# Optimization experiments

Measured on AMD Instinct MI355X. Metric: run time of the kernel, lower is better.

## Reference

```python
import jax, jax.numpy as jnp
import numpy as np

DT = 0.1
TAU = 100.0
ALPHA = DT / TAU


def setup_inputs() -> dict:
    key = jax.random.key(0)
    ks = jax.random.split(key, 4)
    seq_len, batch, in_size, hidden, out_size = 1024, 256, 128, 512, 32
    inputs = jax.random.normal(ks[0], (seq_len, batch, in_size), dtype=jnp.float32)
    W_rec = jax.random.normal(ks[1], (hidden, hidden), dtype=jnp.float32) / hidden ** 0.5
    W_in = jax.random.normal(ks[2], (in_size, hidden), dtype=jnp.float32) / in_size ** 0.5
    b_rec = jnp.zeros((hidden,), dtype=jnp.float32)
    W_out = jax.random.normal(ks[3], (hidden, out_size), dtype=jnp.float32) / hidden ** 0.5
    b_out = jnp.zeros((out_size,), dtype=jnp.float32)
    return {"inputs": inputs, "W_rec": W_rec, "W_in": W_in, "b_rec": b_rec,
            "W_out": W_out, "b_out": b_out}


def reference(inputs, W_rec, W_in, b_rec, W_out, b_out):
    # Precompute input projection for all timesteps: [T, B, H]
    x_proj = jnp.einsum('tbi,ih->tbh', inputs, W_in) + b_rec
    batch, hidden = inputs.shape[1], W_rec.shape[0]
    h0 = jnp.zeros((batch, hidden), dtype=inputs.dtype)

    def step(h, xp_t):
        # h @ W_rec.T matches torch's h @ self.W_rec.t()
        h_new = (1.0 - ALPHA) * h + ALPHA * jax.nn.relu(h @ W_rec.T + xp_t)
        return h_new, h_new

    _, hs = jax.lax.scan(step, h0, x_proj)  # hs: [T, B, H]
    outputs = jnp.einsum('tbh,ho->tbo', hs, W_out) + b_out
    return outputs
```

## Files before the change

### kernel.cpp

```cpp
#include <hip/hip_runtime.h>

typedef __attribute__((ext_vector_type(8))) short short8;
typedef __attribute__((ext_vector_type(4))) float floatx4;

#define T_STEPS 1024
#define BATCH   256
#define INSZ    128
#define HID     512
#define OUTSZ   32

#define MFMA16(a,b,c) __builtin_amdgcn_mfma_f32_16x16x32_bf16((a),(b),(c),0,0,0)

static __device__ __forceinline__ short f2bf(float f) {
  unsigned int u = __float_as_uint(f);
  u += 0x7fffu + ((u >> 16) & 1u);
  return (short)(u >> 16);
}
static __device__ __forceinline__ float bf2f(short s) {
  return __uint_as_float(((unsigned int)(unsigned short)s) << 16);
}
static __device__ __forceinline__ unsigned cvt_pk_bf16(float lo, float hi) {
  unsigned r;
  asm("v_cvt_pk_bf16_f32 %0, %1, %2" : "=v"(r) : "v"(lo), "v"(hi));
  return r;
}

__global__ __launch_bounds__(256) void pack_kernel(
    const float* __restrict__ W_rec, const float* __restrict__ W_in,
    const float* __restrict__ W_out,
    short* __restrict__ w_rec_p, short* __restrict__ w_in_p,
    short* __restrict__ w_out_p) {
  int i = blockIdx.x * 256 + threadIdx.x;
  {
    int n = i >> 9, k = i & 511;
    int pos = ((((k >> 5) * 32 + (n >> 4)) * 64 + ((k >> 3) & 3) * 16 + (n & 15)) << 3) + (k & 7);
    w_rec_p[pos] = f2bf(W_rec[i]);
  }
  if (i < INSZ * HID) {
    int k = i >> 9, n = i & 511;
    int pos = ((((k >> 5) * 32 + (n >> 4)) * 64 + ((k >> 3) & 3) * 16 + (n & 15)) << 3) + (k & 7);
    w_in_p[pos] = f2bf(W_in[i]);
  }
  if (i < HID * OUTSZ) {
    int k = i >> 5, o = i & 31;
    int pos = ((((k >> 5) * 2 + (o >> 4)) * 64 + ((k >> 3) & 3) * 16 + (o & 15)) << 3) + (k & 7);
    w_out_p[pos] = f2bf(W_out[i]);
  }
}

__global__ __launch_bounds__(512, 1) void fused_kernel(
    const float* __restrict__ inputs,
    const short* __restrict__ w_rec_p, const short* __restrict__ w_in_p,
    const short* __restrict__ w_out_p,
    const float* __restrict__ b_rec, const float* __restrict__ b_out,
    short* __restrict__ xp0, short* __restrict__ xp1,
    short* __restrict__ hs0, short* __restrict__ hs1,
    float* __restrict__ h_carry, float* __restrict__ out,
    unsigned long long* __restrict__ xch, unsigned* __restrict__ flags,
    int c, int chunk, int nchunks) {
  __shared__ __align__(16) char smem[163840];
  const int tid  = threadIdx.x;
  const int wave = tid >> 6, lane = tid & 63;
  const int l15  = lane & 15, q = lane >> 4;

  const int sb = (c >= 0 && c < nchunks) ? 32 : 0;
  const int nx = (c + 1 < nchunks) ? chunk : 0;
  const int bid = blockIdx.x;

  if (bid < sb) {
    short* w_lds = (short*)smem;
    short* hbuf  = (short*)(smem + 131072);
    const short* xp = (c & 1) ? xp1 : xp0;
    short* hs = (c & 1) ? hs1 : hs0;
    const int s    = bid;
    const int slab = s >> 1;
    const int ch   = s & 1;
    const int ps   = s ^ 1;
    const int first = (c == 0);

    short8 wreg[8][2];
    #pragma unroll
    for (int kt = 0; kt < 8; ++kt)
      #pragma unroll
      for (int i = 0; i < 2; ++i) {
        int ct = (ch << 4) + wave * 2 + i;
        wreg[kt][i] = *(const short8*)(w_rec_p + (((kt * 32 + ct) * 64 + lane) << 3));
      }

    for (int e = tid * 8; e < 8 * 16 * 512; e += 512 * 8) {
      int kt8 = e >> 13;
      int rest = e & 8191;
      *(short8*)(w_lds + e) =
          *(const short8*)(w_rec_p + ((8 + kt8) * 32 + (ch << 4)) * 512 + rest);
    }

    #pragma unroll
    for (int g4 = 0; g4 < 4; ++g4) {
      int col = (wave * 4 + g4) * 16 + l15;
      int ck = col >> 3, cl = col & 7;
      #pragma unroll
      for (int r = 0; r < 4; ++r) {
        int row = q * 4 + r;
        float v = first ? 0.f : h_carry[(size_t)(slab * 16 + row) * HID + col];
        hbuf[row * 512 + ((ck ^ row) << 3) + cl] = f2bf(v);
      }
    }
    float hold[2][4];
    #pragma unroll
    for (int i = 0; i < 2; ++i) {
      int col = (ch << 8) + wave * 32 + i * 16 + l15;
      #pragma unroll
      for (int r = 0; r < 4; ++r)
        hold[i][r] = first ? 0.f : h_carry[(size_t)(slab * 16 + q * 4 + r) * HID + col];
    }

    const float alpha = (float)(0.1 / 100.0);
    const float onem  = (float)(1.0 - 0.1 / 100.0);

    __syncthreads();

    int p = 0;
    for (int t = 0; t < chunk; ++t) {
      const int g = c * chunk + t;
      const short* hb = hbuf + p * (16 * 512);
      short* hnb = hbuf + (p ^ 1) * (16 * 512);

      uint2 xq[2];
      #pragma unroll
      for (int i = 0; i < 2; ++i)
        xq[i] = *(const uint2*)(xp + ((((size_t)t * 16 + slab) * 32 + (ch << 4) + wave * 2 + i) * 64 + lane) * 4);

      if (t > 0) {
        int e2 = tid * 16;
        int row = e2 >> 9, off = e2 & 511;
        int ck2 = (ch << 5) + (off >> 4);
        short8 v = *(const short8*)(hb + row * 512 + ((ck2 ^ row) << 3));
        *(short8*)(hs + ((size_t)(t - 1) * BATCH + slab * 16 + row) * HID + (ch << 8) + (off >> 1)) = v;
      }

      floatx4 acc[2];
      acc[0] = (floatx4){0.f, 0.f, 0.f, 0.f};
      acc[1] = (floatx4){0.f, 0.f, 0.f, 0.f};

      #pragma unroll
      for (int kt = 0; kt < 8; ++kt) {
        short8 afr = *(const short8*)(hb + l15 * 512 + (((kt * 4 + q) ^ l15) << 3));
        acc[0] = MFMA16(afr, wreg[kt][0], acc[0]);
        acc[1] = MFMA16(afr, wreg[kt][1], acc[1]);
      }
      #pragma unroll
      for (int kt = 8; kt < 16; ++kt) {
        short8 afr = *(const short8*)(hb + l15 * 512 + (((kt * 4 + q) ^ l15) << 3));
        #pragma unroll
        for (int i = 0; i < 2; ++i) {
          short8 bfr = *(const short8*)(w_lds + (kt - 8) * 8192 + (wave * 2 + i) * 512 + lane * 8);
          acc[i] = MFMA16(afr, bfr, acc[i]);
        }
      }

      unsigned long long pk[2];
      #pragma unroll
      for (int i = 0; i < 2; ++i) {
        int col = (ch << 8) + wave * 32 + i * 16 + l15;
        int ck = col >> 3, cl = col & 7;
        float x0 = bf2f((short)(xq[i].x & 0xffffu));
        float x1 = bf2f((short)(xq[i].x >> 16));
        float x2 = bf2f((short)(xq[i].y & 0xffffu));
        float x3 = bf2f((short)(xq[i].y >> 16));
        float h0 = onem * hold[i][0] + alpha * fmaxf(acc[i][0] + x0, 0.f);
        float h1 = onem * hold[i][1] + alpha * fmaxf(acc[i][1] + x1, 0.f);
        float h2 = onem * hold[i][2] + alpha * fmaxf(acc[i][2] + x2, 0.f);
        float h3 = onem * hold[i][3] + alpha * fmaxf(acc[i][3] + x3, 0.f);
        hold[i][0] = h0; hold[i][1] = h1; hold[i][2] = h2; hold[i][3] = h3;
        unsigned u01 = cvt_pk_bf16(h0, h1);
        unsigned u23 = cvt_pk_bf16(h2, h3);
        int r0 = q * 4;
        hnb[(r0 + 0) * 512 + ((ck ^ (r0 + 0)) << 3) + cl] = (short)(u01 & 0xffffu);
        hnb[(r0 + 1) * 512 + ((ck ^ (r0 + 1)) << 3) + cl] = (short)(u01 >> 16);
        hnb[(r0 + 2) * 512 + ((ck ^ (r0 + 2)) << 3) + cl] = (short)(u23 & 0xffffu);
        hnb[(r0 + 3) * 512 + ((ck ^ (r0 + 3)) << 3) + cl] = (short)(u23 >> 16);
        pk[i] = (unsigned long long)u01 | ((unsigned long long)u23 << 32);
      }

      if (t < chunk - 1) {
        unsigned long long* xw = xch + (((size_t)((g + 1) & 1)) * 32 + s) * 1024;
        #pragma unroll
        for (int i = 0; i < 2; ++i) {
          int colLocal = wave * 32 + i * 16 + l15;
          __hip_atomic_store(&xw[colLocal * 4 + q], pk[i],
                             __ATOMIC_RELAXED, __HIP_MEMORY_SCOPE_AGENT);
        }
        asm volatile("s_waitcnt vmcnt(0)" ::: "memory");
        __syncthreads();
        if (tid == 0) {
          __hip_atomic_store(&flags[s], (unsigned)(g + 1),
                             __ATOMIC_RELAXED, __HIP_MEMORY_SCOPE_AGENT);
          unsigned iters = 0;
          while (__hip_atomic_load(&flags[ps], __ATOMIC_RELAXED,
                                   __HIP_MEMORY_SCOPE_AGENT) < (unsigned)(g + 1)) {
            __builtin_amdgcn_s_sleep(1);
            if (++iters > (1u << 27)) break;
          }
        }
        __syncthreads();
        const unsigned long long* xr = xch + (((size_t)((g + 1) & 1)) * 32 + ps) * 1024;
        #pragma unroll
        for (int j = 0; j < 2; ++j) {
          int sIdx = tid * 2 + j;
          unsigned long long v = __hip_atomic_load(&xr[sIdx], __ATOMIC_RELAXED,
                                                   __HIP_MEMORY_SCOPE_AGENT);
          int colLocal = sIdx >> 2, qq = sIdx & 3;
          int col = ((ch ^ 1) << 8) + colLocal;
          int ck = col >> 3, cl = col & 7;
          int r0 = qq * 4;
          hnb[(r0 + 0) * 512 + ((ck ^ (r0 + 0)) << 3) + cl] = (short)(v & 0xffffu);
          hnb[(r0 + 1) * 512 + ((ck ^ (r0 + 1)) << 3) + cl] = (short)((v >> 16) & 0xffffu);
          hnb[(r0 + 2) * 512 + ((ck ^ (r0 + 2)) << 3) + cl] = (short)((v >> 32) & 0xffffu);
          hnb[(r0 + 3) * 512 + ((ck ^ (r0 + 3)) << 3) + cl] = (short)(v >> 48);
        }
        __syncthreads();
      } else {
        __syncthreads();
      }
      p ^= 1;
    }

    {
      const short* hb = hbuf + p * (16 * 512);
      int e2 = tid * 16;
      int row = e2 >> 9, off = e2 & 511;
      int ck2 = (ch << 5) + (off >> 4);
      short8 v = *(const short8*)(hb + row * 512 + ((ck2 ^ row) << 3));
      *(short8*)(hs + ((size_t)(chunk - 1) * BATCH + slab * 16 + row) * HID + (ch << 8) + (off >> 1)) = v;
    }
    #pragma unroll
    for (int i = 0; i < 2; ++i) {
      int col = (ch << 8) + wave * 32 + i * 16 + l15;
      #pragma unroll
      for (int r = 0; r < 4; ++r)
        h_carry[(size_t)(slab * 16 + q * 4 + r) * HID + col] = hold[i][r];
    }

  } else if (bid - sb < nx) {
    const int tt = bid - sb;
    const int cc = c + 1;
    short* xpw = (cc & 1) ? xp1 : xp0;
    const int t_abs = cc * chunk + tt;

    short8 bfr[4][4];
    #pragma unroll
    for (int i = 0; i < 4; ++i)
      #pragma unroll
      for (int kt = 0; kt < 4; ++kt)
        bfr[i][kt] = *(const short8*)(w_in_p + (((kt * 32 + wave * 4 + i) * 64 + lane) << 3));
    float brv[4];
    #pragma unroll
    for (int i = 0; i < 4; ++i) brv[i] = b_rec[(wave * 4 + i) * 16 + l15];

    for (int it = 0; it < 16; ++it) {
      const float* arow = inputs + ((size_t)t_abs * BATCH + it * 16 + l15) * INSZ + q * 8;
      short8 afr[4];
      #pragma unroll
      for (int kt = 0; kt < 4; ++kt) {
        short8 sv;
        #pragma unroll
        for (int j = 0; j < 4; ++j) {
          unsigned u = cvt_pk_bf16(arow[kt * 32 + 2 * j], arow[kt * 32 + 2 * j + 1]);
          sv[2 * j] = (short)(u & 0xffffu);
          sv[2 * j + 1] = (short)(u >> 16);
        }
        afr[kt] = sv;
      }
      floatx4 acc[4];
      #pragma unroll
      for (int i = 0; i < 4; ++i) acc[i] = (floatx4){0.f, 0.f, 0.f, 0.f};
      #pragma unroll
      for (int kt = 0; kt < 4; ++kt)
        #pragma unroll
        for (int i = 0; i < 4; ++i)
          acc[i] = MFMA16(afr[kt], bfr[i][kt], acc[i]);
      #pragma unroll
      for (int i = 0; i < 4; ++i) {
        unsigned u01 = cvt_pk_bf16(acc[i][0] + brv[i], acc[i][1] + brv[i]);
        unsigned u23 = cvt_pk_bf16(acc[i][2] + brv[i], acc[i][3] + brv[i]);
        uint2 u; u.x = u01; u.y = u23;
        *(uint2*)(xpw + ((((size_t)tt * 16 + it) * 32 + wave * 4 + i) * 64 + lane) * 4) = u;
      }
    }

  } else {
    const int tt = bid - sb - nx;
    const int cc = c - 1;
    const short* hsr = (cc & 1) ? hs1 : hs0;
    short* al = (short*)smem + wave * (16 * 520);

    float bov[2] = { b_out[l15], b_out[16 + l15] };

    #pragma unroll
    for (int itm = 0; itm < 2; ++itm) {
      int mt = wave * 2 + itm;
      const short* src = hsr + ((size_t)tt * BATCH + mt * 16) * HID;
      #pragma unroll
      for (int r = 0; r < 16; ++r)
        *(short8*)(al + r * 520 + lane * 8) = *(const short8*)(src + r * 512 + lane * 8);

      floatx4 acc2[2];
      acc2[0] = (floatx4){0.f, 0.f, 0.f, 0.f};
      acc2[1] = (floatx4){0.f, 0.f, 0.f, 0.f};
      #pragma unroll
      for (int kt = 0; kt < 16; ++kt) {
        short8 afr = *(const short8*)(al + l15 * 520 + kt * 32 + q * 8);
        short8 b0 = *(const short8*)(w_out_p + (((kt * 2 + 0) * 64 + lane) << 3));
        short8 b1 = *(const short8*)(w_out_p + (((kt * 2 + 1) * 64 + lane) << 3));
        acc2[0] = MFMA16(afr, b0, acc2[0]);
        acc2[1] = MFMA16(afr, b1, acc2[1]);
      }
      float* outp = out + ((size_t)(cc * chunk + tt) * BATCH + mt * 16) * OUTSZ;
      #pragma unroll
      for (int ot = 0; ot < 2; ++ot)
        #pragma unroll
        for (int r = 0; r < 4; ++r)
          outp[(size_t)(q * 4 + r) * OUTSZ + ot * 16 + l15] = acc2[ot][r] + bov[ot];
    }
  }
}

extern "C" void kernel_launch(void* const* d_in, const int* in_sizes, int n_in,
                              void* d_out, int out_size, void* d_ws, size_t ws_size,
                              hipStream_t stream) {
  const float* inputs = (const float*)d_in[0];
  const float* W_rec  = (const float*)d_in[1];
  const float* W_in   = (const float*)d_in[2];
  const float* b_rec  = (const float*)d_in[3];
  const float* W_out  = (const float*)d_in[4];
  const float* b_out  = (const float*)d_in[5];
  float* out = (float*)d_out;

  char* ws = (char*)d_ws;
  short* w_rec_p = (short*)(ws);
  short* w_in_p  = (short*)(ws + 524288);
  short* w_out_p = (short*)(ws + 655360);
  float* h_carry = (float*)(ws + 688128);
  unsigned long long* xch = (unsigned long long*)(ws + 1200128);
  unsigned* flags = (unsigned*)(ws + 1724416);
  const size_t fixed_end = 2u << 20;

  const size_t per_step = (size_t)BATCH * HID * 2 * 4;
  int chunk = T_STEPS;
  while (chunk > 1 && fixed_end + (size_t)chunk * per_step > ws_size) chunk >>= 1;
  if (fixed_end + (size_t)chunk * per_step > ws_size) return;
  const int nchunks = T_STEPS / chunk;

  const size_t buf = (size_t)chunk * BATCH * HID * 2;
  short* xp0 = (short*)(ws + fixed_end);
  short* xp1 = (short*)(ws + fixed_end + buf);
  short* hs0 = (short*)(ws + fixed_end + 2 * buf);
  short* hs1 = (short*)(ws + fixed_end + 3 * buf);

  hipMemsetAsync(flags, 0, 128, stream);
  pack_kernel<<<1024, 256, 0, stream>>>(W_rec, W_in, W_out, w_rec_p, w_in_p, w_out_p);

  for (int c = -1; c <= nchunks; ++c) {
    int sb = (c >= 0 && c < nchunks) ? 32 : 0;
    int nx = (c + 1 >= 0 && c + 1 < nchunks) ? chunk : 0;
    int no = (c - 1 >= 0 && c - 1 < nchunks) ? chunk : 0;
    int grid = sb + nx + no;
    if (!grid) continue;
    fused_kernel<<<grid, 512, 0, stream>>>(inputs, w_rec_p, w_in_p, w_out_p,
        b_rec, b_out, xp0, xp1, hs0, hs1, h_carry, out, xch, flags,
        c, chunk, nchunks);
  }
}
```

Before: 3.250 ms.

## Overlap partner hidden-state exchange with local-half MFMA in recurrent step

```diff
diff --git a/kernel.cpp b/kernel.cpp
--- a/kernel.cpp
+++ b/kernel.cpp
@@ -55,8 +55,9 @@
     const float* __restrict__ b_rec, const float* __restrict__ b_out,
     short* __restrict__ xp0, short* __restrict__ xp1,
     short* __restrict__ hs0, short* __restrict__ hs1,
-    float* __restrict__ h_carry, float* __restrict__ out,
-    unsigned long long* __restrict__ xch, unsigned* __restrict__ flags,
+    float* __restrict__ h_carry, short* __restrict__ hbc,
+    float* __restrict__ out,
+    short* __restrict__ xch, unsigned* __restrict__ flags,
     int c, int chunk, int nchunks) {
   __shared__ __align__(16) char smem[163840];
   const int tid  = threadIdx.x;
@@ -76,6 +77,7 @@
     const int slab = s >> 1;
     const int ch   = s & 1;
     const int ps   = s ^ 1;
+    const int pch  = ch ^ 1;
     const int first = (c == 0);
 
     short8 wreg[8][2];
@@ -94,24 +96,19 @@
           *(const short8*)(w_rec_p + ((8 + kt8) * 32 + (ch << 4)) * 512 + rest);
     }
 
-    #pragma unroll
-    for (int g4 = 0; g4 < 4; ++g4) {
-      int col = (wave * 4 + g4) * 16 + l15;
-      int ck = col >> 3, cl = col & 7;
+    float hold[2][4];
+    #pragma unroll
+    for (int i = 0; i < 2; ++i) {
+      int colLocal = wave * 32 + i * 16 + l15;
+      int cc = colLocal >> 3, cl = colLocal & 7;
       #pragma unroll
       for (int r = 0; r < 4; ++r) {
         int row = q * 4 + r;
-        float v = first ? 0.f : h_carry[(size_t)(slab * 16 + row) * HID + col];
-        hbuf[row * 512 + ((ck ^ row) << 3) + cl] = f2bf(v);
-      }
-    }
-    float hold[2][4];
-    #pragma unroll
-    for (int i = 0; i < 2; ++i) {
-      int col = (ch << 8) + wave * 32 + i * 16 + l15;
-      #pragma unroll
-      for (int r = 0; r < 4; ++r)
-        hold[i][r] = first ? 0.f : h_carry[(size_t)(slab * 16 + q * 4 + r) * HID + col];
+        float v = first ? 0.f
+                        : h_carry[(size_t)(slab * 16 + row) * HID + (ch << 8) + colLocal];
+        hold[i][r] = v;
+        hbuf[row * 256 + ((cc ^ row) << 3) + cl] = f2bf(v);
+      }
     }
 
     const float alpha = (float)(0.1 / 100.0);
@@ -122,47 +119,76 @@
     int p = 0;
     for (int t = 0; t < chunk; ++t) {
       const int g = c * chunk + t;
-      const short* hb = hbuf + p * (16 * 512);
-      short* hnb = hbuf + (p ^ 1) * (16 * 512);
+      short* hb  = hbuf + p * 4096;
+      short* hnb = hbuf + (p ^ 1) * 4096;
+
+      if (t > 0) {
+        int row = tid >> 5, cc = tid & 31;
+        short8 v = *(const short8*)(hb + row * 256 + ((cc ^ row) << 3));
+        short* slot = xch + (((size_t)(g & 1) * 32 + s) << 12);
+        *(short8*)(slot + row * 256 + cc * 8) = v;
+        *(short8*)(hs + ((size_t)(t - 1) * BATCH + slab * 16 + row) * HID + (ch << 8) + cc * 8) = v;
+        asm volatile("s_waitcnt vmcnt(0)" ::: "memory");
+        __syncthreads();
+        if (tid == 0)
+          __hip_atomic_store(&flags[s], (unsigned)g,
+                             __ATOMIC_RELEASE, __HIP_MEMORY_SCOPE_AGENT);
+      }
 
       uint2 xq[2];
       #pragma unroll
       for (int i = 0; i < 2; ++i)
         xq[i] = *(const uint2*)(xp + ((((size_t)t * 16 + slab) * 32 + (ch << 4) + wave * 2 + i) * 64 + lane) * 4);
-
-      if (t > 0) {
-        int e2 = tid * 16;
-        int row = e2 >> 9, off = e2 & 511;
-        int ck2 = (ch << 5) + (off >> 4);
-        short8 v = *(const short8*)(hb + row * 512 + ((ck2 ^ row) << 3));
-        *(short8*)(hs + ((size_t)(t - 1) * BATCH + slab * 16 + row) * HID + (ch << 8) + (off >> 1)) = v;
-      }
 
       floatx4 acc[2];
       acc[0] = (floatx4){0.f, 0.f, 0.f, 0.f};
       acc[1] = (floatx4){0.f, 0.f, 0.f, 0.f};
 
       #pragma unroll
-      for (int kt = 0; kt < 8; ++kt) {
-        short8 afr = *(const short8*)(hb + l15 * 512 + (((kt * 4 + q) ^ l15) << 3));
-        acc[0] = MFMA16(afr, wreg[kt][0], acc[0]);
-        acc[1] = MFMA16(afr, wreg[kt][1], acc[1]);
-      }
-      #pragma unroll
-      for (int kt = 8; kt < 16; ++kt) {
-        short8 afr = *(const short8*)(hb + l15 * 512 + (((kt * 4 + q) ^ l15) << 3));
-        #pragma unroll
-        for (int i = 0; i < 2; ++i) {
-          short8 bfr = *(const short8*)(w_lds + (kt - 8) * 8192 + (wave * 2 + i) * 512 + lane * 8);
-          acc[i] = MFMA16(afr, bfr, acc[i]);
+      for (int ktrel = 0; ktrel < 8; ++ktrel) {
+        short8 afr = *(const short8*)(hb + l15 * 256 + (((ktrel * 4 + q) ^ l15) << 3));
+        if (ch == 0) {
+          acc[0] = MFMA16(afr, wreg[ktrel][0], acc[0]);
+          acc[1] = MFMA16(afr, wreg[ktrel][1], acc[1]);
+        } else {
+          short8 b0 = *(const short8*)(w_lds + ktrel * 8192 + (wave * 2 + 0) * 512 + lane * 8);
+          short8 b1 = *(const short8*)(w_lds + ktrel * 8192 + (wave * 2 + 1) * 512 + lane * 8);
+          acc[0] = MFMA16(afr, b0, acc[0]);
+          acc[1] = MFMA16(afr, b1, acc[1]);
         }
       }
 
-      unsigned long long pk[2];
+      const short* psrc;
+      if (t == 0) {
+        psrc = hbc + (size_t)(slab * 16) * HID + (pch << 8);
+      } else {
+        unsigned iters = 0;
+        while (__hip_atomic_load(&flags[ps], __ATOMIC_ACQUIRE,
+                                 __HIP_MEMORY_SCOPE_AGENT) < (unsigned)g) {
+          __builtin_amdgcn_s_sleep(2);
+          if (++iters > (1u << 20)) break;
+        }
+        psrc = xch + (((size_t)(g & 1) * 32 + ps) << 12);
+      }
+      const int pstride = (t == 0) ? HID : 256;
+      #pragma unroll
+      for (int ktrel = 0; ktrel < 8; ++ktrel) {
+        short8 afr = *(const short8*)(psrc + l15 * pstride + ktrel * 32 + q * 8);
+        if (ch == 0) {
+          short8 b0 = *(const short8*)(w_lds + ktrel * 8192 + (wave * 2 + 0) * 512 + lane * 8);
+          short8 b1 = *(const short8*)(w_lds + ktrel * 8192 + (wave * 2 + 1) * 512 + lane * 8);
+          acc[0] = MFMA16(afr, b0, acc[0]);
+          acc[1] = MFMA16(afr, b1, acc[1]);
+        } else {
+          acc[0] = MFMA16(afr, wreg[ktrel][0], acc[0]);
+          acc[1] = MFMA16(afr, wreg[ktrel][1], acc[1]);
+        }
+      }
+
       #pragma unroll
       for (int i = 0; i < 2; ++i) {
-        int col = (ch << 8) + wave * 32 + i * 16 + l15;
-        int ck = col >> 3, cl = col & 7;
+        int colLocal = wave * 32 + i * 16 + l15;
+        int cc = colLocal >> 3, cl = colLocal & 7;
         float x0 = bf2f((short)(xq[i].x & 0xffffu));
         float x1 = bf2f((short)(xq[i].x >> 16));
         float x2 = bf2f((short)(xq[i].y & 0xffffu));
@@ -175,70 +201,28 @@
         unsigned u01 = cvt_pk_bf16(h0, h1);
         unsigned u23 = cvt_pk_bf16(h2, h3);
         int r0 = q * 4;
-        hnb[(r0 + 0) * 512 + ((ck ^ (r0 + 0)) << 3) + cl] = (short)(u01 & 0xffffu);
-        hnb[(r0 + 1) * 512 + ((ck ^ (r0 + 1)) << 3) + cl] = (short)(u01 >> 16);
-        hnb[(r0 + 2) * 512 + ((ck ^ (r0 + 2)) << 3) + cl] = (short)(u23 & 0xffffu);
-        hnb[(r0 + 3) * 512 + ((ck ^ (r0 + 3)) << 3) + cl] = (short)(u23 >> 16);
-        pk[i] = (unsigned long long)u01 | ((unsigned long long)u23 << 32);
-      }
-
-      if (t < chunk - 1) {
-        unsigned long long* xw = xch + (((size_t)((g + 1) & 1)) * 32 + s) * 1024;
-        #pragma unroll
-        for (int i = 0; i < 2; ++i) {
-          int colLocal = wave * 32 + i * 16 + l15;
-          __hip_atomic_store(&xw[colLocal * 4 + q], pk[i],
-                             __ATOMIC_RELAXED, __HIP_MEMORY_SCOPE_AGENT);
-        }
-        asm volatile("s_waitcnt vmcnt(0)" ::: "memory");
-        __syncthreads();
-        if (tid == 0) {
-          __hip_atomic_store(&flags[s], (unsigned)(g + 1),
-                             __ATOMIC_RELAXED, __HIP_MEMORY_SCOPE_AGENT);
-          unsigned iters = 0;
-          while (__hip_atomic_load(&flags[ps], __ATOMIC_RELAXED,
-                                   __HIP_MEMORY_SCOPE_AGENT) < (unsigned)(g + 1)) {
-            __builtin_amdgcn_s_sleep(1);
-            if (++iters > (1u << 27)) break;
-          }
-        }
-        __syncthreads();
-        const unsigned long long* xr = xch + (((size_t)((g + 1) & 1)) * 32 + ps) * 1024;
-        #pragma unroll
-        for (int j = 0; j < 2; ++j) {
-          int sIdx = tid * 2 + j;
-          unsigned long long v = __hip_atomic_load(&xr[sIdx], __ATOMIC_RELAXED,
-                                                   __HIP_MEMORY_SCOPE_AGENT);
-          int colLocal = sIdx >> 2, qq = sIdx & 3;
-          int col = ((ch ^ 1) << 8) + colLocal;
-          int ck = col >> 3, cl = col & 7;
-          int r0 = qq * 4;
-          hnb[(r0 + 0) * 512 + ((ck ^ (r0 + 0)) << 3) + cl] = (short)(v & 0xffffu);
-          hnb[(r0 + 1) * 512 + ((ck ^ (r0 + 1)) << 3) + cl] = (short)((v >> 16) & 0xffffu);
-          hnb[(r0 + 2) * 512 + ((ck ^ (r0 + 2)) << 3) + cl] = (short)((v >> 32) & 0xffffu);
-          hnb[(r0 + 3) * 512 + ((ck ^ (r0 + 3)) << 3) + cl] = (short)(v >> 48);
-        }
-        __syncthreads();
-      } else {
-        __syncthreads();
-      }
+        hnb[(r0 + 0) * 256 + ((cc ^ (r0 + 0)) << 3) + cl] = (short)(u01 & 0xffffu);
+        hnb[(r0 + 1) * 256 + ((cc ^ (r0 + 1)) << 3) + cl] = (short)(u01 >> 16);
+        hnb[(r0 + 2) * 256 + ((cc ^ (r0 + 2)) << 3) + cl] = (short)(u23 & 0xffffu);
+        hnb[(r0 + 3) * 256 + ((cc ^ (r0 + 3)) << 3) + cl] = (short)(u23 >> 16);
+      }
+      __syncthreads();
       p ^= 1;
     }
 
     {
-      const short* hb = hbuf + p * (16 * 512);
-      int e2 = tid * 16;
-      int row = e2 >> 9, off = e2 & 511;
-      int ck2 = (ch << 5) + (off >> 4);
-      short8 v = *(const short8*)(hb + row * 512 + ((ck2 ^ row) << 3));
-      *(short8*)(hs + ((size_t)(chunk - 1) * BATCH + slab * 16 + row) * HID + (ch << 8) + (off >> 1)) = v;
+      const short* hb = hbuf + p * 4096;
+      int row = tid >> 5, cc = tid & 31;
+      short8 v = *(const short8*)(hb + row * 256 + ((cc ^ row) << 3));
+      *(short8*)(hs + ((size_t)(chunk - 1) * BATCH + slab * 16 + row) * HID + (ch << 8) + cc * 8) = v;
+      *(short8*)(hbc + (size_t)(slab * 16 + row) * HID + (ch << 8) + cc * 8) = v;
     }
     #pragma unroll
     for (int i = 0; i < 2; ++i) {
-      int col = (ch << 8) + wave * 32 + i * 16 + l15;
+      int colLocal = wave * 32 + i * 16 + l15;
       #pragma unroll
       for (int r = 0; r < 4; ++r)
-        h_carry[(size_t)(slab * 16 + q * 4 + r) * HID + col] = hold[i][r];
+        h_carry[(size_t)(slab * 16 + q * 4 + r) * HID + (ch << 8) + colLocal] = hold[i][r];
     }
 
   } else if (bid - sb < nx) {
@@ -341,8 +325,9 @@
   short* w_in_p  = (short*)(ws + 524288);
   short* w_out_p = (short*)(ws + 655360);
   float* h_carry = (float*)(ws + 688128);
-  unsigned long long* xch = (unsigned long long*)(ws + 1200128);
-  unsigned* flags = (unsigned*)(ws + 1724416);
+  short* xch     = (short*)(ws + 1212416);
+  short* hbc     = (short*)(ws + 1736704);
+  unsigned* flags = (unsigned*)(ws + 1998848);
   const size_t fixed_end = 2u << 20;
 
   const size_t per_step = (size_t)BATCH * HID * 2 * 4;
@@ -358,6 +343,7 @@
   short* hs1 = (short*)(ws + fixed_end + 3 * buf);
 
   hipMemsetAsync(flags, 0, 128, stream);
+  hipMemsetAsync(hbc, 0, (size_t)BATCH * HID * 2, stream);
   pack_kernel<<<1024, 256, 0, stream>>>(W_rec, W_in, W_out, w_rec_p, w_in_p, w_out_p);
 
   for (int c = -1; c <= nchunks; ++c) {
@@ -367,7 +353,7 @@
     int grid = sb + nx + no;
     if (!grid) continue;
     fused_kernel<<<grid, 512, 0, stream>>>(inputs, w_rec_p, w_in_p, w_out_p,
-        b_rec, b_out, xp0, xp1, hs0, hs1, h_carry, out, xch, flags,
+        b_rec, b_out, xp0, xp1, hs0, hs1, h_carry, hbc, out, xch, flags,
         c, chunk, nchunks);
   }
 }
```

Measured after the change: 6.699 ms. 2.06x slower.
